# Performance work log

Measured on AMD Instinct MI355X. Metric: run time of the kernel, lower is better.

The kernel has to match this reference:

```python
import jax, jax.numpy as jnp
import numpy as np

VOCAB, EMBED, HIDDEN = 256, 16, 256
BATCH, SEQ = 128, 512


def setup_inputs() -> dict:
    key = jax.random.key(0)
    ks = jax.random.split(key, 8)
    s = lambda fan_in: 1.0 / np.sqrt(fan_in)
    return {
        "x": jax.random.randint(ks[0], (BATCH, SEQ), 0, VOCAB, dtype=jnp.int32),
        "embed": jax.random.normal(ks[1], (VOCAB, EMBED), dtype=jnp.float32),
        "W_ih": jax.random.uniform(ks[2], (EMBED, 3 * HIDDEN), jnp.float32, -s(EMBED), s(EMBED)),
        "b_ih": jax.random.uniform(ks[3], (3 * HIDDEN,), jnp.float32, -s(EMBED), s(EMBED)),
        "W_hh": jax.random.uniform(ks[4], (HIDDEN, 3 * HIDDEN), jnp.float32, -s(HIDDEN), s(HIDDEN)),
        "b_hh": jax.random.uniform(ks[5], (3 * HIDDEN,), jnp.float32, -s(HIDDEN), s(HIDDEN)),
        "W_out": jax.random.uniform(ks[6], (HIDDEN, VOCAB), jnp.float32, -s(HIDDEN), s(HIDDEN)),
        "b_out": jax.random.uniform(ks[7], (VOCAB,), jnp.float32, -s(HIDDEN), s(HIDDEN)),
    }


def reference(x, embed, W_ih, b_ih, W_hh, b_hh, W_out, b_out):
    B = x.shape[0]
    H = W_hh.shape[0]
    emb = embed[x]                                   # [B, S, E]
    # input-side gate pre-activations can be batched across time (same math)
    gi = jnp.einsum("bse,eg->bsg", emb, W_ih) + b_ih  # [B, S, 3H]

    def step(h, gi_t):
        gh = h @ W_hh + b_hh                          # [B, 3H]
        r_i, z_i, n_i = jnp.split(gi_t, 3, axis=-1)
        r_h, z_h, n_h = jnp.split(gh, 3, axis=-1)
        r = jax.nn.sigmoid(r_i + r_h)
        z = jax.nn.sigmoid(z_i + z_h)
        n = jnp.tanh(n_i + r * n_h)
        h_new = (1.0 - z) * n + z * h
        return h_new, h_new

    h0 = jnp.zeros((B, H), dtype=emb.dtype)
    _, hs = jax.lax.scan(step, h0, jnp.swapaxes(gi, 0, 1))  # hs: [S, B, H]
    h_seq = jnp.swapaxes(hs, 0, 1)                           # [B, S, H]
    return jnp.einsum("bsh,hv->bsv", h_seq, W_out) + b_out   # [B, S, V]
```

## Files before the change

### kernel.cpp

```cpp
#include <hip/hip_runtime.h>
#include <hip/hip_fp16.h>

#define BB 128
#define SS 512
#define EE 16
#define HH 256
#define G3 768
#define VV 256

typedef _Float16 half8 __attribute__((ext_vector_type(8)));
typedef _Float16 half4_t __attribute__((ext_vector_type(4)));
typedef float f32x4 __attribute__((ext_vector_type(4)));

__global__ __launch_bounds__(256) void swizzle_weights(
    const float* __restrict__ Whh, const float* __restrict__ Wout,
    _Float16* __restrict__ whh_swz, _Float16* __restrict__ wout_swz) {
  int t = blockIdx.x * 256 + threadIdx.x;
  if (t < 48 * 8 * 64 * 8) {
    int j = t & 7, L = (t >> 3) & 63, k = (t >> 9) & 7, n = t >> 12;
    int row = k * 32 + (L >> 4) * 8 + j;
    int col = n * 16 + (L & 15);
    whh_swz[t] = (_Float16)Whh[row * G3 + col];
  }
  if (t < 16 * 8 * 64 * 8) {
    int j = t & 7, L = (t >> 3) & 63, k = (t >> 9) & 7, n = t >> 12;
    int row = k * 32 + (L >> 4) * 8 + j;
    int col = n * 16 + (L & 15);
    wout_swz[t] = (_Float16)Wout[row * VV + col];
  }
}

__global__ __launch_bounds__(256) void gi_kernel(
    const int* __restrict__ x, const float* __restrict__ embed,
    const float* __restrict__ W_ih, const float* __restrict__ b_ih,
    const float* __restrict__ b_hh, _Float16* __restrict__ gi_swz) {
  int gid = blockIdx.x;
  int bg = gid >> 7;
  int t0 = (gid & 127) * 4;
  int tid = threadIdx.x;

  __shared__ __align__(16) float s_wih[EE * G3];
  __shared__ __align__(16) float s_bias[G3];
  __shared__ __align__(16) float s_emb16[4][16][EE];
  __shared__ int s_x[4][16];

  for (int i = tid; i < EE * G3; i += 256) s_wih[i] = W_ih[i];
  for (int i = tid; i < G3; i += 256)
    s_bias[i] = b_ih[i] + (i < 512 ? b_hh[i] : 0.0f);
  if (tid < 64) {
    int tt = tid >> 4, m = tid & 15;
    s_x[tt][m] = x[(bg * 16 + m) * SS + t0 + tt];
  }
  __syncthreads();
  for (int i = tid; i < 4 * 16 * EE; i += 256) {
    int tt = i >> 8, m = (i >> 4) & 15, e = i & 15;
    s_emb16[tt][m][e] = embed[s_x[tt][m] * EE + e];
  }
  __syncthreads();

  for (int cch = 0; cch < 3; cch++) {
    int gc = cch * 256 + tid;
    float w[EE];
#pragma unroll
    for (int e = 0; e < EE; e++) w[e] = s_wih[e * G3 + gc];
    float bias = s_bias[gc];
    int wi = (gc >> 4) & 15, cc = gc & 15;
    int tilebase = (cch * 16 + wi) * 64;
    for (int tt = 0; tt < 4; tt++) {
      size_t gbase = (size_t)(bg * 512 + t0 + tt) * 12288;
#pragma unroll
      for (int mq = 0; mq < 4; mq++) {
        half4_t v;
#pragma unroll
        for (int r = 0; r < 4; r++) {
          int m = mq * 4 + r;
          float acc = bias;
#pragma unroll
          for (int e = 0; e < EE; e++) acc += s_emb16[tt][m][e] * w[e];
          v[r] = (_Float16)acc;
        }
        *(half4_t*)(gi_swz + gbase + (size_t)((tilebase + mq * 16 + cc) * 4)) = v;
      }
    }
  }
}

__global__ void __launch_bounds__(1024)
__attribute__((amdgpu_waves_per_eu(4, 4)))
gru_kernel(
    const _Float16* __restrict__ gi_swz, const _Float16* __restrict__ whh_swz,
    const float* __restrict__ b_hh, _Float16* __restrict__ h_seq) {
  int bg = blockIdx.x;
  int tid = threadIdx.x;
  int w = tid >> 6, L = tid & 63;
  int q = L >> 4, c = L & 15;

  __shared__ __align__(16) _Float16 s_h[2][16][264];

  half8 wR[8], wZ[8], wN[8];
#pragma unroll
  for (int k = 0; k < 8; k++) {
    wR[k] = *(const half8*)(whh_swz + (((size_t)((0 * 16 + w) * 8 + k) * 64 + L) * 8));
    wZ[k] = *(const half8*)(whh_swz + (((size_t)((1 * 16 + w) * 8 + k) * 64 + L) * 8));
    wN[k] = *(const half8*)(whh_swz + (((size_t)((2 * 16 + w) * 8 + k) * 64 + L) * 8));
  }
  float bhn = b_hh[512 + w * 16 + c];

  for (int idx = tid; idx < (2 * 16 * 264) / 2; idx += 1024)
    ((unsigned int*)s_h)[idx] = 0u;
  __syncthreads();

  int col = w * 16 + c;
  unsigned hoff = (unsigned)(bg * 16 + q * 4) * (SS * HH) + (unsigned)col;
  unsigned gioff = (unsigned)(bg * 512) * 12288u + (unsigned)((w * 64 + L) * 4);

  int cur = 0;
#pragma unroll 1
  for (int t = 0; t < SS; t++) {
    half4_t giR = *(const half4_t*)(gi_swz + gioff);
    half4_t giZ = *(const half4_t*)(gi_swz + gioff + 4096u);
    half4_t giN = *(const half4_t*)(gi_swz + gioff + 8192u);

    const _Float16* hsrc = &s_h[cur][0][0];
    half4_t hp;
#pragma unroll
    for (int r = 0; r < 4; r++) hp[r] = hsrc[(q * 4 + r) * 264 + col];

    f32x4 aR = {0.f, 0.f, 0.f, 0.f}, aZ = aR, aN = aR;
#pragma unroll
    for (int k = 0; k < 8; k++) {
      half8 av = *(const half8*)(hsrc + c * 264 + k * 32 + q * 8);
      aR = __builtin_amdgcn_mfma_f32_16x16x32_f16(av, wR[k], aR, 0, 0, 0);
      aZ = __builtin_amdgcn_mfma_f32_16x16x32_f16(av, wZ[k], aZ, 0, 0, 0);
      aN = __builtin_amdgcn_mfma_f32_16x16x32_f16(av, wN[k], aN, 0, 0, 0);
    }

    _Float16* hdst = &s_h[cur ^ 1][0][0];
#pragma unroll
    for (int r = 0; r < 4; r++) {
      int m = q * 4 + r;
      float rg = aR[r] + (float)giR[r];
      rg = 1.f / (1.f + __expf(-rg));
      float zg = aZ[r] + (float)giZ[r];
      zg = 1.f / (1.f + __expf(-zg));
      float ng = (float)giN[r] + rg * (aN[r] + bhn);
      ng = 2.f / (1.f + __expf(-2.f * ng)) - 1.f;
      float hn = (1.f - zg) * ng + zg * (float)hp[r];
      hdst[m * 264 + col] = (_Float16)hn;
      h_seq[(size_t)hoff + (unsigned)r * (SS * HH)] = (_Float16)hn;
    }
    __syncthreads();
    cur ^= 1;
    hoff += HH;
    gioff += 12288u;
  }
}

__global__ __launch_bounds__(256) void out_kernel(
    const _Float16* __restrict__ h_seq, const _Float16* __restrict__ wout_swz,
    const float* __restrict__ b_out, float* __restrict__ out) {
  int blk = blockIdx.x;
  int tid = threadIdx.x;
  int w = tid >> 6, L = tid & 63, q = L >> 4, c = L & 15;

  __shared__ __align__(16) _Float16 s_a[64 * 264];

  const _Float16* src = h_seq + (size_t)blk * 64 * 256;
  for (int idx = tid; idx < (64 * 256) / 8; idx += 256) {
    int row = idx >> 5, kk = (idx & 31) * 8;
    *(half8*)(s_a + row * 264 + kk) = *(const half8*)(src + row * 256 + kk);
  }
  __syncthreads();

  half8 a[8];
#pragma unroll
  for (int k = 0; k < 8; k++)
    a[k] = *(const half8*)(s_a + (w * 16 + c) * 264 + k * 32 + q * 8);

  f32x4 acc[16];
#pragma unroll
  for (int n = 0; n < 16; n++) {
    f32x4 z = {0.f, 0.f, 0.f, 0.f};
    acc[n] = z;
#pragma unroll
    for (int k = 0; k < 8; k++) {
      half8 b = *(const half8*)(wout_swz + ((size_t)(n * 8 + k) * 64 + L) * 8);
      acc[n] = __builtin_amdgcn_mfma_f32_16x16x32_f16(a[k], b, acc[n], 0, 0, 0);
    }
  }
#pragma unroll
  for (int n = 0; n < 16; n++) {
    int v = n * 16 + c;
    float bo = b_out[v];
#pragma unroll
    for (int r = 0; r < 4; r++) {
      int bt = blk * 64 + w * 16 + q * 4 + r;
      out[(size_t)bt * 256 + v] = acc[n][r] + bo;
    }
  }
}

extern "C" void kernel_launch(void* const* d_in, const int* in_sizes, int n_in,
                              void* d_out, int out_size, void* d_ws, size_t ws_size,
                              hipStream_t stream) {
  const int*   x    = (const int*)d_in[0];
  const float* emb  = (const float*)d_in[1];
  const float* Wih  = (const float*)d_in[2];
  const float* bih  = (const float*)d_in[3];
  const float* Whh  = (const float*)d_in[4];
  const float* bhh  = (const float*)d_in[5];
  const float* Wout = (const float*)d_in[6];
  const float* bout = (const float*)d_in[7];

  char* ws = (char*)d_ws;
  _Float16* gi_swz   = (_Float16*)(ws);
  _Float16* whh_swz  = (_Float16*)(ws + 100663296);
  _Float16* wout_swz = (_Float16*)(ws + 100663296 + 393216);
  _Float16* h_seq    = (_Float16*)(ws + 100663296 + 393216 + 131072);

  swizzle_weights<<<768, 256, 0, stream>>>(Whh, Wout, whh_swz, wout_swz);
  gi_kernel<<<1024, 256, 0, stream>>>(x, emb, Wih, bih, bhh, gi_swz);
  gru_kernel<<<8, 1024, 0, stream>>>(gi_swz, whh_swz, bhh, h_seq);
  out_kernel<<<1024, 256, 0, stream>>>(h_seq, wout_swz, bout, (float*)d_out);
}
```

Measured before the change: 1.574 ms.

## Halve GRU block to 8 waves, each computing two column tiles

The recurrent GRU kernel now runs 512 threads per block instead of 1024. Each wave keeps two 16-column tiles of W_hh in registers and issues six MFMA chains per k-step, reusing each loaded A fragment across both tiles. The previous h values are also kept in registers rather than reread from LDS. The aim is cheaper per-step barrier synchronisation and fewer LDS reads on the serial critical path. The cost is higher register pressure (192 VGPRs of weights) and more serial MFMA and elementwise work per wave.

After: 1.778 ms. 1.13x slower.

```diff
diff --git a/kernel.cpp b/kernel.cpp
--- a/kernel.cpp
+++ b/kernel.cpp
@@ -85,8 +85,8 @@
   }
 }
 
-__global__ void __launch_bounds__(1024)
-__attribute__((amdgpu_waves_per_eu(4, 4)))
+__global__ void __launch_bounds__(512)
+__attribute__((amdgpu_waves_per_eu(2, 2)))
 gru_kernel(
     const _Float16* __restrict__ gi_swz, const _Float16* __restrict__ whh_swz,
     const float* __restrict__ b_hh, _Float16* __restrict__ h_seq) {
@@ -97,62 +97,89 @@
 
   __shared__ __align__(16) _Float16 s_h[2][16][264];
 
-  half8 wR[8], wZ[8], wN[8];
-#pragma unroll
-  for (int k = 0; k < 8; k++) {
-    wR[k] = *(const half8*)(whh_swz + (((size_t)((0 * 16 + w) * 8 + k) * 64 + L) * 8));
-    wZ[k] = *(const half8*)(whh_swz + (((size_t)((1 * 16 + w) * 8 + k) * 64 + L) * 8));
-    wN[k] = *(const half8*)(whh_swz + (((size_t)((2 * 16 + w) * 8 + k) * 64 + L) * 8));
-  }
-  float bhn = b_hh[512 + w * 16 + c];
-
-  for (int idx = tid; idx < (2 * 16 * 264) / 2; idx += 1024)
+  half8 wB[2][3][8];
+#pragma unroll
+  for (int n = 0; n < 2; n++)
+#pragma unroll
+    for (int g = 0; g < 3; g++)
+#pragma unroll
+      for (int k = 0; k < 8; k++)
+        wB[n][g][k] = *(const half8*)(
+            whh_swz + (((size_t)((g * 16 + (2 * w + n)) * 8 + k) * 64 + L) * 8));
+
+  float bhn0 = b_hh[512 + w * 32 + c];
+  float bhn1 = b_hh[512 + w * 32 + 16 + c];
+
+  for (int idx = tid; idx < (2 * 16 * 264) / 2; idx += 512)
     ((unsigned int*)s_h)[idx] = 0u;
   __syncthreads();
 
-  int col = w * 16 + c;
-  unsigned hoff = (unsigned)(bg * 16 + q * 4) * (SS * HH) + (unsigned)col;
-  unsigned gioff = (unsigned)(bg * 512) * 12288u + (unsigned)((w * 64 + L) * 4);
-
-  int cur = 0;
+  half4_t hp0 = {(_Float16)0.f, (_Float16)0.f, (_Float16)0.f, (_Float16)0.f};
+  half4_t hp1 = hp0;
+
+  unsigned hoff = (unsigned)(bg * 16 + q * 4) * (SS * HH) + (unsigned)(w * 32 + c);
+  unsigned gio = (unsigned)(bg * 512) * 12288u + (unsigned)(w * 512 + L * 4);
+
+  _Float16* hsrc = &s_h[0][0][0];
+  _Float16* hdst = &s_h[1][0][0];
+  const int aoff = c * 264 + q * 8;
+  const int woff = (q * 4) * 264 + w * 32 + c;
+
 #pragma unroll 1
   for (int t = 0; t < SS; t++) {
-    half4_t giR = *(const half4_t*)(gi_swz + gioff);
-    half4_t giZ = *(const half4_t*)(gi_swz + gioff + 4096u);
-    half4_t giN = *(const half4_t*)(gi_swz + gioff + 8192u);
-
-    const _Float16* hsrc = &s_h[cur][0][0];
-    half4_t hp;
-#pragma unroll
-    for (int r = 0; r < 4; r++) hp[r] = hsrc[(q * 4 + r) * 264 + col];
-
-    f32x4 aR = {0.f, 0.f, 0.f, 0.f}, aZ = aR, aN = aR;
+    half4_t gR0 = *(const half4_t*)(gi_swz + gio);
+    half4_t gR1 = *(const half4_t*)(gi_swz + gio + 256u);
+    half4_t gZ0 = *(const half4_t*)(gi_swz + gio + 4096u);
+    half4_t gZ1 = *(const half4_t*)(gi_swz + gio + 4352u);
+    half4_t gN0 = *(const half4_t*)(gi_swz + gio + 8192u);
+    half4_t gN1 = *(const half4_t*)(gi_swz + gio + 8448u);
+
+    f32x4 aR0 = {0.f, 0.f, 0.f, 0.f}, aZ0 = aR0, aN0 = aR0;
+    f32x4 aR1 = aR0, aZ1 = aR0, aN1 = aR0;
 #pragma unroll
     for (int k = 0; k < 8; k++) {
-      half8 av = *(const half8*)(hsrc + c * 264 + k * 32 + q * 8);
-      aR = __builtin_amdgcn_mfma_f32_16x16x32_f16(av, wR[k], aR, 0, 0, 0);
-      aZ = __builtin_amdgcn_mfma_f32_16x16x32_f16(av, wZ[k], aZ, 0, 0, 0);
-      aN = __builtin_amdgcn_mfma_f32_16x16x32_f16(av, wN[k], aN, 0, 0, 0);
-    }
-
-    _Float16* hdst = &s_h[cur ^ 1][0][0];
+      half8 av = *(const half8*)(hsrc + aoff + k * 32);
+      aR0 = __builtin_amdgcn_mfma_f32_16x16x32_f16(av, wB[0][0][k], aR0, 0, 0, 0);
+      aZ0 = __builtin_amdgcn_mfma_f32_16x16x32_f16(av, wB[0][1][k], aZ0, 0, 0, 0);
+      aN0 = __builtin_amdgcn_mfma_f32_16x16x32_f16(av, wB[0][2][k], aN0, 0, 0, 0);
+      aR1 = __builtin_amdgcn_mfma_f32_16x16x32_f16(av, wB[1][0][k], aR1, 0, 0, 0);
+      aZ1 = __builtin_amdgcn_mfma_f32_16x16x32_f16(av, wB[1][1][k], aZ1, 0, 0, 0);
+      aN1 = __builtin_amdgcn_mfma_f32_16x16x32_f16(av, wB[1][2][k], aN1, 0, 0, 0);
+    }
+
 #pragma unroll
     for (int r = 0; r < 4; r++) {
-      int m = q * 4 + r;
-      float rg = aR[r] + (float)giR[r];
-      rg = 1.f / (1.f + __expf(-rg));
-      float zg = aZ[r] + (float)giZ[r];
-      zg = 1.f / (1.f + __expf(-zg));
-      float ng = (float)giN[r] + rg * (aN[r] + bhn);
-      ng = 2.f / (1.f + __expf(-2.f * ng)) - 1.f;
-      float hn = (1.f - zg) * ng + zg * (float)hp[r];
-      hdst[m * 264 + col] = (_Float16)hn;
-      h_seq[(size_t)hoff + (unsigned)r * (SS * HH)] = (_Float16)hn;
+      {
+        float rg = aR0[r] + (float)gR0[r];
+        rg = 1.f / (1.f + __expf(-rg));
+        float zg = aZ0[r] + (float)gZ0[r];
+        zg = 1.f / (1.f + __expf(-zg));
+        float ng = (float)gN0[r] + rg * (aN0[r] + bhn0);
+        ng = 2.f / (1.f + __expf(-2.f * ng)) - 1.f;
+        float hn = (1.f - zg) * ng + zg * (float)hp0[r];
+        _Float16 h16 = (_Float16)hn;
+        hp0[r] = h16;
+        hdst[woff + r * 264] = h16;
+        h_seq[(size_t)(hoff + (unsigned)r * 131072u)] = h16;
+      }
+      {
+        float rg = aR1[r] + (float)gR1[r];
+        rg = 1.f / (1.f + __expf(-rg));
+        float zg = aZ1[r] + (float)gZ1[r];
+        zg = 1.f / (1.f + __expf(-zg));
+        float ng = (float)gN1[r] + rg * (aN1[r] + bhn1);
+        ng = 2.f / (1.f + __expf(-2.f * ng)) - 1.f;
+        float hn = (1.f - zg) * ng + zg * (float)hp1[r];
+        _Float16 h16 = (_Float16)hn;
+        hp1[r] = h16;
+        hdst[woff + r * 264 + 16] = h16;
+        h_seq[(size_t)(hoff + (unsigned)r * 131072u + 16u)] = h16;
+      }
     }
     __syncthreads();
-    cur ^= 1;
-    hoff += HH;
-    gioff += 12288u;
+    _Float16* tp = hsrc; hsrc = hdst; hdst = tp;
+    gio += 12288u;
+    hoff += (unsigned)HH;
   }
 }
 
@@ -220,6 +247,6 @@
 
   swizzle_weights<<<768, 256, 0, stream>>>(Whh, Wout, whh_swz, wout_swz);
   gi_kernel<<<1024, 256, 0, stream>>>(x, emb, Wih, bih, bhh, gi_swz);
-  gru_kernel<<<8, 1024, 0, stream>>>(gi_swz, whh_swz, bhh, h_seq);
+  gru_kernel<<<8, 512, 0, stream>>>(gi_swz, whh_swz, bhh, h_seq);
   out_kernel<<<1024, 256, 0, stream>>>(h_seq, wout_swz, bout, (float*)d_out);
 }
```

## Prefetch next-step gate inputs and streamline GRU recurrence loop

Applied to the files above, without the earlier changes.

The GRU loop now loads the next timestep's input gate pre-activations one iteration ahead, so global-load latency overlaps the current step's MFMA work. The gate inputs and the hidden bias seed the MFMA accumulators directly, the previous hidden state stays in registers instead of being reread from LDS, and __syncthreads is replaced by an explicit lgkmcnt wait plus s_barrier. The h_seq global stores move after the barrier so they stay off the critical path. This adds register pressure and relies on hand-managed waitcnt semantics for correctness.

Result: slower. 1.983 ms (+26.0%).

```diff
diff --git a/kernel.cpp b/kernel.cpp
--- a/kernel.cpp
+++ b/kernel.cpp
@@ -110,49 +110,68 @@
     ((unsigned int*)s_h)[idx] = 0u;
   __syncthreads();
 
+  half4_t hp = {(_Float16)0.f, (_Float16)0.f, (_Float16)0.f, (_Float16)0.f};
+
   int col = w * 16 + c;
   unsigned hoff = (unsigned)(bg * 16 + q * 4) * (SS * HH) + (unsigned)col;
-  unsigned gioff = (unsigned)(bg * 512) * 12288u + (unsigned)((w * 64 + L) * 4);
-
-  int cur = 0;
+  unsigned gio = (unsigned)(bg * 512) * 12288u + (unsigned)((w * 64 + L) * 4);
+
+  half4_t nR = *(const half4_t*)(gi_swz + gio);
+  half4_t nZ = *(const half4_t*)(gi_swz + gio + 4096u);
+  half4_t nN = *(const half4_t*)(gi_swz + gio + 8192u);
+
+  const _Float16* hsrc = &s_h[0][0][0];
+  _Float16* hdst = &s_h[1][0][0];
+  const int aoff = c * 264 + q * 8;
+  const int woff = (q * 4) * 264 + col;
+
 #pragma unroll 1
   for (int t = 0; t < SS; t++) {
-    half4_t giR = *(const half4_t*)(gi_swz + gioff);
-    half4_t giZ = *(const half4_t*)(gi_swz + gioff + 4096u);
-    half4_t giN = *(const half4_t*)(gi_swz + gioff + 8192u);
-
-    const _Float16* hsrc = &s_h[cur][0][0];
-    half4_t hp;
-#pragma unroll
-    for (int r = 0; r < 4; r++) hp[r] = hsrc[(q * 4 + r) * 264 + col];
-
-    f32x4 aR = {0.f, 0.f, 0.f, 0.f}, aZ = aR, aN = aR;
+    f32x4 aR, aZ, aN;
+#pragma unroll
+    for (int r = 0; r < 4; r++) {
+      aR[r] = (float)nR[r];
+      aZ[r] = (float)nZ[r];
+      aN[r] = bhn;
+    }
+    half4_t giN = nN;
+
+    gio += 12288u;
+    nR = *(const half4_t*)(gi_swz + gio);
+    nZ = *(const half4_t*)(gi_swz + gio + 4096u);
+    nN = *(const half4_t*)(gi_swz + gio + 8192u);
+
 #pragma unroll
     for (int k = 0; k < 8; k++) {
-      half8 av = *(const half8*)(hsrc + c * 264 + k * 32 + q * 8);
+      half8 av = *(const half8*)(hsrc + aoff + k * 32);
       aR = __builtin_amdgcn_mfma_f32_16x16x32_f16(av, wR[k], aR, 0, 0, 0);
       aZ = __builtin_amdgcn_mfma_f32_16x16x32_f16(av, wZ[k], aZ, 0, 0, 0);
       aN = __builtin_amdgcn_mfma_f32_16x16x32_f16(av, wN[k], aN, 0, 0, 0);
     }
 
-    _Float16* hdst = &s_h[cur ^ 1][0][0];
+    half4_t h16v;
 #pragma unroll
     for (int r = 0; r < 4; r++) {
-      int m = q * 4 + r;
-      float rg = aR[r] + (float)giR[r];
-      rg = 1.f / (1.f + __expf(-rg));
-      float zg = aZ[r] + (float)giZ[r];
-      zg = 1.f / (1.f + __expf(-zg));
-      float ng = (float)giN[r] + rg * (aN[r] + bhn);
+      float rg = 1.f / (1.f + __expf(-aR[r]));
+      float zg = 1.f / (1.f + __expf(-aZ[r]));
+      float ng = (float)giN[r] + rg * aN[r];
       ng = 2.f / (1.f + __expf(-2.f * ng)) - 1.f;
       float hn = (1.f - zg) * ng + zg * (float)hp[r];
-      hdst[m * 264 + col] = (_Float16)hn;
-      h_seq[(size_t)hoff + (unsigned)r * (SS * HH)] = (_Float16)hn;
-    }
-    __syncthreads();
-    cur ^= 1;
-    hoff += HH;
-    gioff += 12288u;
+      _Float16 h16 = (_Float16)hn;
+      hp[r] = h16;
+      h16v[r] = h16;
+      hdst[woff + r * 264] = h16;
+    }
+
+    asm volatile("s_waitcnt lgkmcnt(0)" ::: "memory");
+    __builtin_amdgcn_s_barrier();
+
+#pragma unroll
+    for (int r = 0; r < 4; r++)
+      h_seq[(size_t)(hoff + (unsigned)r * 131072u)] = h16v[r];
+
+    const _Float16* tp = hsrc; hsrc = hdst; hdst = (_Float16*)tp;
+    hoff += (unsigned)HH;
   }
 }
 
```
